# Optimization experiments

Measured on AMD Instinct MI355X. Metric: run time of the kernel, lower is better.

Reference implementation:

```python
import jax, jax.numpy as jnp
import numpy as np

N_AGENT = 60000
N_MAP = 40000
N = N_AGENT + N_MAP
E = 3200000
HID = 32
PERIODS = 30
PRED = 50


def setup_inputs() -> dict:
    key = jax.random.key(0)
    ks = jax.random.split(key, 20)
    def w(k, shape, s=0.1):
        return jax.random.normal(k, shape, jnp.float32) * s
    return {
        "agent_x": jax.random.normal(ks[0], (N_AGENT, 9), jnp.float32),
        "map_x": jax.random.normal(ks[1], (N_MAP, 6), jnp.float32),
        "edge_index": jax.random.randint(ks[2], (2, E), 0, N),
        "W_agent": w(ks[3], (9, HID)), "b_agent": jnp.zeros((HID,), jnp.float32),
        "W_map": w(ks[4], (6, HID)), "b_map": jnp.zeros((HID,), jnp.float32),
        # TGCN cell: three GCNConvs (z, r, h gates) + three Linear(2*HID -> HID)
        "Wz_c": w(ks[5], (HID, HID)), "bz_c": jnp.zeros((HID,), jnp.float32),
        "Wr_c": w(ks[6], (HID, HID)), "br_c": jnp.zeros((HID,), jnp.float32),
        "Wh_c": w(ks[7], (HID, HID)), "bh_c": jnp.zeros((HID,), jnp.float32),
        "Wz_l": w(ks[8], (2 * HID, HID)), "bz_l": jnp.zeros((HID,), jnp.float32),
        "Wr_l": w(ks[9], (2 * HID, HID)), "br_l": jnp.zeros((HID,), jnp.float32),
        "Wh_l": w(ks[10], (2 * HID, HID)), "bh_l": jnp.zeros((HID,), jnp.float32),
        "attn": w(ks[11], (PERIODS,), 1.0),
        "W1": w(ks[12], (HID, 2 * HID)), "b1": jnp.zeros((2 * HID,), jnp.float32),
        "W2": w(ks[13], (2 * HID, 2 * PRED)), "b2": jnp.zeros((2 * PRED,), jnp.float32),
    }


def reference(agent_x, map_x, edge_index, W_agent, b_agent, W_map, b_map,
              Wz_c, bz_c, Wr_c, br_c, Wh_c, bh_c,
              Wz_l, bz_l, Wr_l, br_l, Wh_l, bh_l,
              attn, W1, b1, W2, b2):
    n = agent_x.shape[0] + map_x.shape[0]
    # encoders + concat map nodes after agent nodes
    x = jnp.concatenate([agent_x @ W_agent + b_agent,
                         map_x @ W_map + b_map], axis=0)  # [N, HID]

    # GCN normalization with self-loops: A_hat = D^-1/2 (A + I) D^-1/2
    loop = jnp.arange(n, dtype=edge_index.dtype)
    src = jnp.concatenate([edge_index[0], loop])
    dst = jnp.concatenate([edge_index[1], loop])
    deg = jax.ops.segment_sum(jnp.ones(src.shape[0], jnp.float32), dst, num_segments=n)
    dinv = jnp.where(deg > 0, jax.lax.rsqrt(deg), 0.0)
    norm = dinv[src] * dinv[dst]  # [E + N]

    def gcn(W, b):
        m = (x @ W)[src] * norm[:, None]          # gather + scale: [E+N, HID]
        return jax.ops.segment_sum(m, dst, num_segments=n) + b

    zeros_h = jnp.zeros_like(x)  # hidden state H = 0 (A3TGCN never threads H)
    z = jax.nn.sigmoid(jnp.concatenate([gcn(Wz_c, bz_c), zeros_h], 1) @ Wz_l + bz_l)
    r = jax.nn.sigmoid(jnp.concatenate([gcn(Wr_c, br_c), zeros_h], 1) @ Wr_l + br_l)
    h_tilde = jnp.tanh(jnp.concatenate([gcn(Wh_c, bh_c), zeros_h * r], 1) @ Wh_l + bh_l)
    h_new = (1.0 - z) * h_tilde  # z*H + (1-z)*h_tilde with H=0

    # attention-weighted sum over periods; every period is identical so it
    # collapses to sum(softmax(attn)) * h_new (== h_new, kept for fidelity)
    probs = jax.nn.softmax(attn)
    h_acc = jnp.sum(probs) * h_new

    h = jax.nn.relu(h_acc)[:agent_x.shape[0]]     # keep agent nodes only
    pred = jax.nn.relu(h @ W1 + b1) @ W2 + b2     # [num_agents, 2*PRED]
    return pred.reshape(-1, PRED, 2)
```

## Files before the change

kernel.cpp:

```cpp
#include <hip/hip_runtime.h>
#include <hip/hip_fp16.h>
#include <math.h>

#define N_AGENT 60000
#define N_MAP   40000
#define N_NODES 100000
#define NE      3200000
#define HID     32
#define PERIODS 30

#define NBUCK   391
#define NABUCK  235
#define CAP     10240
#define TILE    4096
#define PTHREADS 512
#define ABLK    128
#define GEBLK   8192

__global__ void k_precompute(const float* Wz_c, const float* bz_c,
                             const float* Wh_c, const float* bh_c,
                             const float* Wz_l, const float* bz_l,
                             const float* Wh_l, const float* bh_l,
                             const float* attn,
                             float* Mz, float* Mh, float* bz_eff, float* bh_eff,
                             float* s_out, int* cursor) {
    int t = threadIdx.x;
    int k = t >> 5, c = t & 31;
    float mz = 0.f, mh = 0.f;
    for (int j = 0; j < HID; ++j) {
        mz += Wz_c[k * HID + j] * Wz_l[j * HID + c];
        mh += Wh_c[k * HID + j] * Wh_l[j * HID + c];
    }
    Mz[t] = mz; Mh[t] = mh;
    if (t < NBUCK) cursor[t] = t * CAP;
    if (t < HID) {
        float bz = bz_l[t], bh = bh_l[t];
        for (int j = 0; j < HID; ++j) {
            bz += bz_c[j] * Wz_l[j * HID + t];
            bh += bh_c[j] * Wh_l[j * HID + t];
        }
        bz_eff[t] = bz; bh_eff[t] = bh;
    }
    if (t == 0) {
        float m = -1e30f;
        for (int i = 0; i < PERIODS; ++i) m = fmaxf(m, attn[i]);
        float S = 0.f;
        for (int i = 0; i < PERIODS; ++i) S += expf(attn[i] - m);
        float s = 0.f;
        for (int i = 0; i < PERIODS; ++i) s += expf(attn[i] - m) / S;
        *s_out = s;
    }
}

__global__ __launch_bounds__(PTHREADS) void k_partition(
        const int* __restrict__ src, const int* __restrict__ dst,
        int* __restrict__ cursor, int* __restrict__ ebuf) {
    __shared__ int sCnt[NBUCK];
    __shared__ int sBase[NBUCK + 1];
    __shared__ int sGbase[NBUCK];
    __shared__ int sScan[PTHREADS];
    __shared__ int sReorder[TILE];
    int t = threadIdx.x;
    int tileBase = blockIdx.x * TILE;
    int tcount = NE - tileBase; if (tcount > TILE) tcount = TILE;

    if (t < NBUCK) sCnt[t] = 0;
    __syncthreads();

    int pb[8], pp[8], pr[8];
    const int4* s4 = (const int4*)src;
    const int4* d4 = (const int4*)dst;
#pragma unroll
    for (int k = 0; k < 2; ++k) {
        int e4 = (tileBase >> 2) + t + k * PTHREADS;
        int valid = (e4 << 2) < NE;
        int4 sv, dv;
        if (valid) { sv = s4[e4]; dv = d4[e4]; }
#define PROC(m, SS, DD) { int kk = k * 4 + m;                                  \
        if (valid) { pb[kk] = (DD) >> 8;                                       \
                     pp[kk] = (SS) | (((DD) & 255) << 17);                     \
                     pr[kk] = atomicAdd(&sCnt[pb[kk]], 1); }                   \
        else pb[kk] = -1; }
        PROC(0, sv.x, dv.x)
        PROC(1, sv.y, dv.y)
        PROC(2, sv.z, dv.z)
        PROC(3, sv.w, dv.w)
#undef PROC
    }
    __syncthreads();

    int v = (t < NBUCK) ? sCnt[t] : 0;
    sScan[t] = v;
    __syncthreads();
    for (int s = 1; s < PTHREADS; s <<= 1) {
        int a = (t >= s) ? sScan[t - s] : 0;
        __syncthreads();
        sScan[t] += a;
        __syncthreads();
    }
    if (t <= NBUCK) sBase[t] = sScan[t] - v;
    __syncthreads();
    if (t < NBUCK && sCnt[t] > 0) sGbase[t] = atomicAdd(&cursor[t], sCnt[t]);
    __syncthreads();
#pragma unroll
    for (int k = 0; k < 8; ++k) {
        if (pb[k] >= 0) sReorder[sBase[pb[k]] + pr[k]] = pp[k];
    }
    __syncthreads();
#pragma unroll
    for (int k = 0; k < 8; ++k) {
        int j = t + k * PTHREADS;
        if (j < tcount) {
            int lo = 0, hi = NBUCK;
            while (hi - lo > 1) {
                int m = (lo + hi) >> 1;
                if (sBase[m] <= j) lo = m; else hi = m;
            }
            ebuf[sGbase[lo] + (j - sBase[lo])] = sReorder[j];
        }
    }
}

__global__ __launch_bounds__(256) void k_hist(const int* __restrict__ cursor,
                                              const int* __restrict__ ebuf,
                                              int* __restrict__ deg,
                                              int* __restrict__ qdeg) {
    __shared__ int h[1024];
    int t = threadIdx.x;
    int b = blockIdx.x;
    for (int j = t; j < 1024; j += 256) h[j] = 0;
    __syncthreads();
    int start = b * CAP;
    int cnt = cursor[b] - start;
    for (int j = t; j < cnt; j += 256) {
        int p = ebuf[start + j];
        int dl = (p >> 17) & 255;
        int s = p & 0x1FFFF;
        int qt = (s >= 25000) + (s >= 50000) + (s >= 75000);
        atomicAdd(&h[dl * 4 + qt], 1);
    }
    __syncthreads();
    int node = b * 256 + t;
    if (node < N_NODES)
        deg[node] = h[t * 4] + h[t * 4 + 1] + h[t * 4 + 2] + h[t * 4 + 3];
    for (int j = t; j < 1024; j += 256) {
        int q4 = b * 1024 + j;
        if (q4 < N_NODES * 4) qdeg[q4] = h[j];
    }
}

__global__ void k_encode(const float* __restrict__ agent_x, const float* __restrict__ map_x,
                         const float* __restrict__ W_agent, const float* __restrict__ b_agent,
                         const float* __restrict__ W_map, const float* __restrict__ b_map,
                         const int* __restrict__ deg,
                         __half* __restrict__ y_h) {
    int t = blockIdx.x * blockDim.x + threadIdx.x;
    if (t >= (N_NODES + 1) * HID) return;
    int i = t >> 5, c = t & 31;
    float acc = 0.f;
    if (i < N_AGENT) {
        float v = (c < 9) ? agent_x[(size_t)i * 9 + c] : 0.f;
        acc = b_agent[c];
#pragma unroll
        for (int k = 0; k < 9; ++k) acc += __shfl(v, k, 32) * W_agent[k * HID + c];
        acc *= rsqrtf((float)deg[i] + 1.0f);
    } else if (i < N_NODES) {
        float v = (c < 6) ? map_x[(size_t)(i - N_AGENT) * 6 + c] : 0.f;
        acc = b_map[c];
#pragma unroll
        for (int k = 0; k < 6; ++k) acc += __shfl(v, k, 32) * W_map[k * HID + c];
        acc *= rsqrtf((float)deg[i] + 1.0f);
    }
    y_h[t] = __float2half(acc);
}

__global__ __launch_bounds__(1024) void k_sortlocal(
        const int* __restrict__ cursor, int* __restrict__ ebuf,
        const int* __restrict__ qdeg, int* __restrict__ row_start) {
    __shared__ int sSorted[CAP];
    __shared__ int sBase[1024];
    __shared__ int sCnt[1024];
    __shared__ int sScan[1024];
    int t = threadIdx.x;
    const int b = blockIdx.x;

    int v = qdeg[b * 1024 + t];
    sCnt[t] = 0;
    sScan[t] = v;
    __syncthreads();
    for (int st = 1; st < 1024; st <<= 1) {
        int a = (t >= st) ? sScan[t - st] : 0;
        __syncthreads();
        sScan[t] += a;
        __syncthreads();
    }
    sBase[t] = sScan[t] - v;
    if ((t & 3) == 0) row_start[b * 256 + (t >> 2)] = b * CAP + sBase[t];
    __syncthreads();

    const int start = b * CAP;
    const int cnt = cursor[b] - start;
    for (int j = t; j < cnt; j += 1024) {
        int p = ebuf[start + j];
        int dl = (p >> 17) & 255;
        int s = p & 0x1FFFF;
        int qt = (s >= 25000) + (s >= 50000) + (s >= 75000);
        int bin = dl * 4 + qt;
        int r = atomicAdd(&sCnt[bin], 1);
        sSorted[sBase[bin] + r] = s;
    }
    __syncthreads();
    for (int j = t; j < cnt; j += 1024)
        ebuf[start + j] = sSorted[j];
}

__global__ __launch_bounds__(1024) void k_agg(
        const int* __restrict__ row_start, const int* __restrict__ deg,
        const int* __restrict__ ebuf, const __half* __restrict__ y_h,
        float* __restrict__ h_pre) {
    __shared__ int sEdge[GEBLK];
    __shared__ int sOff[ABLK + 1];
    int t = threadIdx.x;
    const int nodeBase = blockIdx.x * ABLK;

    if (t < ABLK) sOff[t] = row_start[nodeBase + t];
    if (t == ABLK) {
        int last = nodeBase + ABLK - 1;
        sOff[ABLK] = row_start[last] + deg[last];
    }
    __syncthreads();

    const int e_begin = sOff[0];
    const int cnt = sOff[ABLK] - e_begin;
    for (int j = t; j < cnt && j < GEBLK; j += 1024) sEdge[j] = ebuf[e_begin + j];
    __syncthreads();

    const int lane = t & 63;
    const int r = (t >> 6) * 8 + (lane >> 3);
    const int q = lane & 7;
    const int i = nodeBase + r;
    const uint2* yh2 = (const uint2*)y_h;

    if (i < N_AGENT) {
        float ax = 0.f, ay = 0.f, az = 0.f, aw = 0.f;
        if (cnt <= GEBLK) {
            int e0 = sOff[r] - e_begin, e1 = sOff[r + 1] - e_begin;
            for (int j = e0; j < e1; j += 8) {
                uint2 v[8];
#pragma unroll
                for (int u = 0; u < 8; ++u) {
                    int idx = (j + u < e1) ? sEdge[j + u] : N_NODES;
                    v[u] = yh2[(size_t)idx * 8 + q];
                }
#pragma unroll
                for (int u = 0; u < 8; ++u) {
                    __half2 h0 = *reinterpret_cast<__half2*>(&v[u].x);
                    __half2 h1 = *reinterpret_cast<__half2*>(&v[u].y);
                    float2 f0 = __half22float2(h0);
                    float2 f1 = __half22float2(h1);
                    ax += f0.x; ay += f0.y; az += f1.x; aw += f1.y;
                }
            }
        } else {
            int e0 = sOff[r], e1 = sOff[r + 1];
            for (int j = e0; j < e1; j += 8) {
                uint2 v[8];
#pragma unroll
                for (int u = 0; u < 8; ++u) {
                    int idx = (j + u < e1) ? ebuf[j + u] : N_NODES;
                    v[u] = yh2[(size_t)idx * 8 + q];
                }
#pragma unroll
                for (int u = 0; u < 8; ++u) {
                    __half2 h0 = *reinterpret_cast<__half2*>(&v[u].x);
                    __half2 h1 = *reinterpret_cast<__half2*>(&v[u].y);
                    float2 f0 = __half22float2(h0);
                    float2 f1 = __half22float2(h1);
                    ax += f0.x; ay += f0.y; az += f1.x; aw += f1.y;
                }
            }
        }
        *(float4*)&h_pre[(size_t)i * HID + q * 4] = make_float4(ax, ay, az, aw);
    }
}

__global__ __launch_bounds__(256) void k_mlp(
        const int* __restrict__ deg, const float* __restrict__ h_pre,
        const __half* __restrict__ y_h,
        const float* __restrict__ Mz, const float* __restrict__ Mh,
        const float* __restrict__ bz_eff, const float* __restrict__ bh_eff,
        const float* __restrict__ s_ptr,
        const float* __restrict__ W1, const float* __restrict__ b1,
        const float* __restrict__ W2, const float* __restrict__ b2,
        float* __restrict__ out) {
    int n = blockIdx.x * 256 + threadIdx.x;
    if (n >= N_AGENT) return;
    const float s = *s_ptr;
    float di = rsqrtf((float)deg[n] + 1.0f);

    float a[32];
    const float4* hp4 = (const float4*)(h_pre + (size_t)n * HID);
    const uint2*  sh2 = (const uint2*)(y_h + (size_t)n * HID);
#pragma unroll
    for (int u = 0; u < 8; ++u) {
        float4 hv = hp4[u];
        uint2 sv = sh2[u];
        __half2 s0 = *reinterpret_cast<const __half2*>(&sv.x);
        __half2 s1 = *reinterpret_cast<const __half2*>(&sv.y);
        float2 f0 = __half22float2(s0);
        float2 f1 = __half22float2(s1);
        a[u * 4 + 0] = (hv.x + f0.x) * di;
        a[u * 4 + 1] = (hv.y + f0.y) * di;
        a[u * 4 + 2] = (hv.z + f1.x) * di;
        a[u * 4 + 3] = (hv.w + f1.y) * di;
    }

    float hv32[32];
#pragma unroll
    for (int cc = 0; cc < 4; ++cc) {
        float uz[8], uh[8];
#pragma unroll
        for (int j = 0; j < 8; ++j) { uz[j] = bz_eff[cc * 8 + j]; uh[j] = bh_eff[cc * 8 + j]; }
#pragma unroll
        for (int k = 0; k < 32; ++k) {
#pragma unroll
            for (int j = 0; j < 8; ++j) {
                uz[j] += a[k] * Mz[k * 32 + cc * 8 + j];
                uh[j] += a[k] * Mh[k * 32 + cc * 8 + j];
            }
        }
#pragma unroll
        for (int j = 0; j < 8; ++j) {
            float z = 1.0f / (1.0f + expf(-uz[j]));
            float hh = s * (1.0f - z) * tanhf(uh[j]);
            hv32[cc * 8 + j] = fmaxf(hh, 0.0f);
        }
    }

    float tv[64];
#pragma unroll
    for (int tc = 0; tc < 8; ++tc) {
        float acc[8];
#pragma unroll
        for (int j = 0; j < 8; ++j) acc[j] = b1[tc * 8 + j];
#pragma unroll
        for (int k = 0; k < 32; ++k) {
#pragma unroll
            for (int j = 0; j < 8; ++j)
                acc[j] += hv32[k] * W1[k * 64 + tc * 8 + j];
        }
#pragma unroll
        for (int j = 0; j < 8; ++j) tv[tc * 8 + j] = fmaxf(acc[j], 0.0f);
    }

    float* orow = out + (size_t)n * 100;
    for (int oc = 0; oc < 13; ++oc) {
        int cbase = oc * 8; if (cbase > 92) cbase = 92;
        float acc[8];
#pragma unroll
        for (int j = 0; j < 8; ++j) acc[j] = b2[cbase + j];
#pragma unroll
        for (int k = 0; k < 64; ++k) {
#pragma unroll
            for (int j = 0; j < 8; ++j)
                acc[j] += tv[k] * W2[k * 100 + cbase + j];
        }
#pragma unroll
        for (int j = 0; j < 8; ++j) orow[cbase + j] = acc[j];
    }
}

extern "C" void kernel_launch(void* const* d_in, const int* in_sizes, int n_in,
                              void* d_out, int out_size, void* d_ws, size_t ws_size,
                              hipStream_t stream) {
    const float* agent_x = (const float*)d_in[0];
    const float* map_x   = (const float*)d_in[1];
    const int*   ei      = (const int*)d_in[2];
    const float* W_agent = (const float*)d_in[3];
    const float* b_agent = (const float*)d_in[4];
    const float* W_map   = (const float*)d_in[5];
    const float* b_map   = (const float*)d_in[6];
    const float* Wz_c    = (const float*)d_in[7];
    const float* bz_c    = (const float*)d_in[8];
    const float* Wh_c    = (const float*)d_in[11];
    const float* bh_c    = (const float*)d_in[12];
    const float* Wz_l    = (const float*)d_in[13];
    const float* bz_l    = (const float*)d_in[14];
    const float* Wh_l    = (const float*)d_in[17];
    const float* bh_l    = (const float*)d_in[18];
    const float* attn    = (const float*)d_in[19];
    const float* W1      = (const float*)d_in[20];
    const float* b1      = (const float*)d_in[21];
    const float* W2      = (const float*)d_in[22];
    const float* b2      = (const float*)d_in[23];
    float* out = (float*)d_out;

    const int* e_src = ei;
    const int* e_dst = ei + NE;

    float*  ws       = (float*)d_ws;
    __half* y_h      = (__half*)ws;
    float*  Mz       = ws + 1600128;
    float*  Mh       = ws + 1601152;
    float*  bz       = ws + 1602176;
    float*  bh       = ws + 1602208;
    float*  sS       = ws + 1602240;
    int*    deg      = (int*)(ws + 1602304);
    int*    cursor   = (int*)(ws + 1702400);
    int*    row_start= (int*)(ws + 1702912);
    int*    qdeg     = (int*)(ws + 1763328);
    float*  h_pre    = ws + 2163328;
    int*    ebuf     = (int*)(ws + 4088448);

    k_precompute<<<1, 1024, 0, stream>>>(Wz_c, bz_c, Wh_c, bh_c, Wz_l, bz_l,
                                         Wh_l, bh_l, attn, Mz, Mh, bz, bh, sS, cursor);
    k_partition<<<(NE + TILE - 1) / TILE, PTHREADS, 0, stream>>>(e_src, e_dst, cursor, ebuf);
    k_hist<<<NBUCK, 256, 0, stream>>>(cursor, ebuf, deg, qdeg);
    k_encode<<<((N_NODES + 1) * HID + 255) / 256, 256, 0, stream>>>(
        agent_x, map_x, W_agent, b_agent, W_map, b_map, deg, y_h);
    k_sortlocal<<<NABUCK, 1024, 0, stream>>>(cursor, ebuf, qdeg, row_start);
    k_agg<<<(N_AGENT + ABLK - 1) / ABLK, 1024, 0, stream>>>(
        row_start, deg, ebuf, y_h, h_pre);
    k_mlp<<<(N_AGENT + 255) / 256, 256, 0, stream>>>(
        deg, h_pre, y_h, Mz, Mh, bz, bh, sS, W1, b1, W2, b2, out);
}
```

Measured before the change: 311.6 us.

## Fuse neighbor aggregation with gate and output MLP using 8-lane shuffles

Merges the aggregation and MLP kernels into one. Each group of 8 lanes that aggregated a node's 32 features now computes that node's gates, hidden layer and 100 outputs cooperatively, exchanging values with width-8 shuffles. This removes the h_pre round trip through global memory and one launch, and replaces the register-heavy one-thread-per-node MLP with work split across lanes. In exchange the MLP now runs inside the 1024-thread aggregation kernel, which may raise register pressure and lower occupancy for the gather phase. The degree is now taken from row offsets rather than the deg array.

```diff
diff --git a/kernel.cpp b/kernel.cpp
--- a/kernel.cpp
+++ b/kernel.cpp
@@ -214,160 +214,140 @@
         ebuf[start + j] = sSorted[j];
 }
 
-__global__ __launch_bounds__(1024) void k_agg(
+__global__ __launch_bounds__(1024) void k_aggmlp(
         const int* __restrict__ row_start, const int* __restrict__ deg,
         const int* __restrict__ ebuf, const __half* __restrict__ y_h,
-        float* __restrict__ h_pre) {
-    __shared__ int sEdge[GEBLK];
-    __shared__ int sOff[ABLK + 1];
-    int t = threadIdx.x;
-    const int nodeBase = blockIdx.x * ABLK;
-
-    if (t < ABLK) sOff[t] = row_start[nodeBase + t];
-    if (t == ABLK) {
-        int last = nodeBase + ABLK - 1;
-        sOff[ABLK] = row_start[last] + deg[last];
-    }
-    __syncthreads();
-
-    const int e_begin = sOff[0];
-    const int cnt = sOff[ABLK] - e_begin;
-    for (int j = t; j < cnt && j < GEBLK; j += 1024) sEdge[j] = ebuf[e_begin + j];
-    __syncthreads();
-
-    const int lane = t & 63;
-    const int r = (t >> 6) * 8 + (lane >> 3);
-    const int q = lane & 7;
-    const int i = nodeBase + r;
-    const uint2* yh2 = (const uint2*)y_h;
-
-    if (i < N_AGENT) {
-        float ax = 0.f, ay = 0.f, az = 0.f, aw = 0.f;
-        if (cnt <= GEBLK) {
-            int e0 = sOff[r] - e_begin, e1 = sOff[r + 1] - e_begin;
-            for (int j = e0; j < e1; j += 8) {
-                uint2 v[8];
-#pragma unroll
-                for (int u = 0; u < 8; ++u) {
-                    int idx = (j + u < e1) ? sEdge[j + u] : N_NODES;
-                    v[u] = yh2[(size_t)idx * 8 + q];
-                }
-#pragma unroll
-                for (int u = 0; u < 8; ++u) {
-                    __half2 h0 = *reinterpret_cast<__half2*>(&v[u].x);
-                    __half2 h1 = *reinterpret_cast<__half2*>(&v[u].y);
-                    float2 f0 = __half22float2(h0);
-                    float2 f1 = __half22float2(h1);
-                    ax += f0.x; ay += f0.y; az += f1.x; aw += f1.y;
-                }
-            }
-        } else {
-            int e0 = sOff[r], e1 = sOff[r + 1];
-            for (int j = e0; j < e1; j += 8) {
-                uint2 v[8];
-#pragma unroll
-                for (int u = 0; u < 8; ++u) {
-                    int idx = (j + u < e1) ? ebuf[j + u] : N_NODES;
-                    v[u] = yh2[(size_t)idx * 8 + q];
-                }
-#pragma unroll
-                for (int u = 0; u < 8; ++u) {
-                    __half2 h0 = *reinterpret_cast<__half2*>(&v[u].x);
-                    __half2 h1 = *reinterpret_cast<__half2*>(&v[u].y);
-                    float2 f0 = __half22float2(h0);
-                    float2 f1 = __half22float2(h1);
-                    ax += f0.x; ay += f0.y; az += f1.x; aw += f1.y;
-                }
-            }
-        }
-        *(float4*)&h_pre[(size_t)i * HID + q * 4] = make_float4(ax, ay, az, aw);
-    }
-}
-
-__global__ __launch_bounds__(256) void k_mlp(
-        const int* __restrict__ deg, const float* __restrict__ h_pre,
-        const __half* __restrict__ y_h,
         const float* __restrict__ Mz, const float* __restrict__ Mh,
         const float* __restrict__ bz_eff, const float* __restrict__ bh_eff,
         const float* __restrict__ s_ptr,
         const float* __restrict__ W1, const float* __restrict__ b1,
         const float* __restrict__ W2, const float* __restrict__ b2,
         float* __restrict__ out) {
-    int n = blockIdx.x * 256 + threadIdx.x;
-    if (n >= N_AGENT) return;
-    const float s = *s_ptr;
-    float di = rsqrtf((float)deg[n] + 1.0f);
-
-    float a[32];
-    const float4* hp4 = (const float4*)(h_pre + (size_t)n * HID);
-    const uint2*  sh2 = (const uint2*)(y_h + (size_t)n * HID);
-#pragma unroll
-    for (int u = 0; u < 8; ++u) {
-        float4 hv = hp4[u];
-        uint2 sv = sh2[u];
-        __half2 s0 = *reinterpret_cast<const __half2*>(&sv.x);
-        __half2 s1 = *reinterpret_cast<const __half2*>(&sv.y);
+    __shared__ int sEdge[GEBLK];
+    __shared__ int sOff[ABLK + 1];
+    int t = threadIdx.x;
+    const int nodeBase = blockIdx.x * ABLK;
+
+    if (t < ABLK) sOff[t] = row_start[nodeBase + t];
+    if (t == ABLK) {
+        int last = nodeBase + ABLK - 1;
+        sOff[ABLK] = row_start[last] + deg[last];
+    }
+    __syncthreads();
+
+    const int e_begin = sOff[0];
+    const int cnt = sOff[ABLK] - e_begin;
+    for (int j = t; j < cnt && j < GEBLK; j += 1024) sEdge[j] = ebuf[e_begin + j];
+    __syncthreads();
+
+    const int lane = t & 63;
+    const int r = (t >> 6) * 8 + (lane >> 3);
+    const int q = lane & 7;
+    const int i = nodeBase + r;
+    const uint2* yh2 = (const uint2*)y_h;
+
+    if (i >= N_AGENT) return;
+
+    float ax = 0.f, ay = 0.f, az = 0.f, aw = 0.f;
+    int e0g = sOff[r], e1g = sOff[r + 1];
+    if (cnt <= GEBLK) {
+        int e0 = e0g - e_begin, e1 = e1g - e_begin;
+        for (int j = e0; j < e1; j += 8) {
+            uint2 v[8];
+#pragma unroll
+            for (int u = 0; u < 8; ++u) {
+                int idx = (j + u < e1) ? sEdge[j + u] : N_NODES;
+                v[u] = yh2[(size_t)idx * 8 + q];
+            }
+#pragma unroll
+            for (int u = 0; u < 8; ++u) {
+                __half2 h0 = *reinterpret_cast<__half2*>(&v[u].x);
+                __half2 h1 = *reinterpret_cast<__half2*>(&v[u].y);
+                float2 f0 = __half22float2(h0);
+                float2 f1 = __half22float2(h1);
+                ax += f0.x; ay += f0.y; az += f1.x; aw += f1.y;
+            }
+        }
+    } else {
+        for (int j = e0g; j < e1g; j += 8) {
+            uint2 v[8];
+#pragma unroll
+            for (int u = 0; u < 8; ++u) {
+                int idx = (j + u < e1g) ? ebuf[j + u] : N_NODES;
+                v[u] = yh2[(size_t)idx * 8 + q];
+            }
+#pragma unroll
+            for (int u = 0; u < 8; ++u) {
+                __half2 h0 = *reinterpret_cast<__half2*>(&v[u].x);
+                __half2 h1 = *reinterpret_cast<__half2*>(&v[u].y);
+                float2 f0 = __half22float2(h0);
+                float2 f1 = __half22float2(h1);
+                ax += f0.x; ay += f0.y; az += f1.x; aw += f1.y;
+            }
+        }
+    }
+
+    const float di = rsqrtf((float)(e1g - e0g) + 1.0f);
+    float a[4];
+    {
+        uint2 sv = yh2[(size_t)i * 8 + q];
+        __half2 s0 = *reinterpret_cast<__half2*>(&sv.x);
+        __half2 s1 = *reinterpret_cast<__half2*>(&sv.y);
         float2 f0 = __half22float2(s0);
         float2 f1 = __half22float2(s1);
-        a[u * 4 + 0] = (hv.x + f0.x) * di;
-        a[u * 4 + 1] = (hv.y + f0.y) * di;
-        a[u * 4 + 2] = (hv.z + f1.x) * di;
-        a[u * 4 + 3] = (hv.w + f1.y) * di;
-    }
-
-    float hv32[32];
-#pragma unroll
-    for (int cc = 0; cc < 4; ++cc) {
-        float uz[8], uh[8];
-#pragma unroll
-        for (int j = 0; j < 8; ++j) { uz[j] = bz_eff[cc * 8 + j]; uh[j] = bh_eff[cc * 8 + j]; }
-#pragma unroll
-        for (int k = 0; k < 32; ++k) {
-#pragma unroll
-            for (int j = 0; j < 8; ++j) {
-                uz[j] += a[k] * Mz[k * 32 + cc * 8 + j];
-                uh[j] += a[k] * Mh[k * 32 + cc * 8 + j];
-            }
+        a[0] = (ax + f0.x) * di;
+        a[1] = (ay + f0.y) * di;
+        a[2] = (az + f1.x) * di;
+        a[3] = (aw + f1.y) * di;
+    }
+
+    const float s = *s_ptr;
+    float uz[4], uh[4];
+#pragma unroll
+    for (int j = 0; j < 4; ++j) { uz[j] = bz_eff[q * 4 + j]; uh[j] = bh_eff[q * 4 + j]; }
+#pragma unroll
+    for (int k = 0; k < 32; ++k) {
+        float ak = __shfl(a[k & 3], k >> 2, 8);
+#pragma unroll
+        for (int j = 0; j < 4; ++j) {
+            uz[j] += ak * Mz[k * 32 + q * 4 + j];
+            uh[j] += ak * Mh[k * 32 + q * 4 + j];
         }
-#pragma unroll
-        for (int j = 0; j < 8; ++j) {
-            float z = 1.0f / (1.0f + expf(-uz[j]));
-            float hh = s * (1.0f - z) * tanhf(uh[j]);
-            hv32[cc * 8 + j] = fmaxf(hh, 0.0f);
-        }
-    }
-
-    float tv[64];
-#pragma unroll
-    for (int tc = 0; tc < 8; ++tc) {
-        float acc[8];
-#pragma unroll
-        for (int j = 0; j < 8; ++j) acc[j] = b1[tc * 8 + j];
-#pragma unroll
-        for (int k = 0; k < 32; ++k) {
-#pragma unroll
-            for (int j = 0; j < 8; ++j)
-                acc[j] += hv32[k] * W1[k * 64 + tc * 8 + j];
-        }
-#pragma unroll
-        for (int j = 0; j < 8; ++j) tv[tc * 8 + j] = fmaxf(acc[j], 0.0f);
-    }
-
-    float* orow = out + (size_t)n * 100;
-    for (int oc = 0; oc < 13; ++oc) {
-        int cbase = oc * 8; if (cbase > 92) cbase = 92;
-        float acc[8];
-#pragma unroll
-        for (int j = 0; j < 8; ++j) acc[j] = b2[cbase + j];
-#pragma unroll
-        for (int k = 0; k < 64; ++k) {
-#pragma unroll
-            for (int j = 0; j < 8; ++j)
-                acc[j] += tv[k] * W2[k * 100 + cbase + j];
-        }
-#pragma unroll
-        for (int j = 0; j < 8; ++j) orow[cbase + j] = acc[j];
-    }
+    }
+    float hv[4];
+#pragma unroll
+    for (int j = 0; j < 4; ++j) {
+        float z = 1.0f / (1.0f + expf(-uz[j]));
+        hv[j] = fmaxf(s * (1.0f - z) * tanhf(uh[j]), 0.0f);
+    }
+
+    float tv[8];
+#pragma unroll
+    for (int j = 0; j < 8; ++j) tv[j] = b1[q * 8 + j];
+#pragma unroll
+    for (int k = 0; k < 32; ++k) {
+        float hk = __shfl(hv[k & 3], k >> 2, 8);
+#pragma unroll
+        for (int j = 0; j < 8; ++j)
+            tv[j] += hk * W1[k * 64 + q * 8 + j];
+    }
+#pragma unroll
+    for (int j = 0; j < 8; ++j) tv[j] = fmaxf(tv[j], 0.0f);
+
+    const int cbase = (q == 7) ? 87 : q * 13;
+    float o[13];
+#pragma unroll
+    for (int j = 0; j < 13; ++j) o[j] = b2[cbase + j];
+#pragma unroll
+    for (int k = 0; k < 64; ++k) {
+        float tk = __shfl(tv[k & 7], k >> 3, 8);
+#pragma unroll
+        for (int j = 0; j < 13; ++j)
+            o[j] += tk * W2[k * 100 + cbase + j];
+    }
+    float* orow = out + (size_t)i * 100;
+#pragma unroll
+    for (int j = 0; j < 13; ++j) orow[cbase + j] = o[j];
 }
 
 extern "C" void kernel_launch(void* const* d_in, const int* in_sizes, int n_in,
@@ -409,8 +389,7 @@
     int*    cursor   = (int*)(ws + 1702400);
     int*    row_start= (int*)(ws + 1702912);
     int*    qdeg     = (int*)(ws + 1763328);
-    float*  h_pre    = ws + 2163328;
-    int*    ebuf     = (int*)(ws + 4088448);
+    int*    ebuf     = (int*)(ws + 2163328);
 
     k_precompute<<<1, 1024, 0, stream>>>(Wz_c, bz_c, Wh_c, bh_c, Wz_l, bz_l,
                                          Wh_l, bh_l, attn, Mz, Mh, bz, bh, sS, cursor);
@@ -419,8 +398,6 @@
     k_encode<<<((N_NODES + 1) * HID + 255) / 256, 256, 0, stream>>>(
         agent_x, map_x, W_agent, b_agent, W_map, b_map, deg, y_h);
     k_sortlocal<<<NABUCK, 1024, 0, stream>>>(cursor, ebuf, qdeg, row_start);
-    k_agg<<<(N_AGENT + ABLK - 1) / ABLK, 1024, 0, stream>>>(
-        row_start, deg, ebuf, y_h, h_pre);
-    k_mlp<<<(N_AGENT + 255) / 256, 256, 0, stream>>>(
-        deg, h_pre, y_h, Mz, Mh, bz, bh, sS, W1, b1, W2, b2, out);
-}
+    k_aggmlp<<<(N_AGENT + ABLK - 1) / ABLK, 1024, 0, stream>>>(
+        row_start, deg, ebuf, y_h, Mz, Mh, bz, bh, sS, W1, b1, W2, b2, out);
+}
```

Measured after the change: 444.1 us. 1.43x slower.
